# Performance work log

Measured on AMD Instinct MI355X. Metric: run time of the kernel, lower is better.

## Reference

```python
import jax, jax.numpy as jnp
import numpy as np

H, W, D, HEADS = 32, 32, 16, 8
EPS = 1e-5

def _ln(x, g, b):
    m = jnp.mean(x, -1, keepdims=True)
    v = jnp.mean((x - m) ** 2, -1, keepdims=True)
    return (x - m) / jnp.sqrt(v + EPS) * g + b

def _attn(x, w_qkv, w_proj, b_proj):
    # x: (Bb, N, C); torch Linear: y = x @ W.T + b
    Bb, N, C = x.shape
    hd = C // HEADS
    qkv = jnp.einsum('bnc,dc->bnd', x, w_qkv).reshape(Bb, N, 3, HEADS, hd)
    q, k, v = qkv[:, :, 0], qkv[:, :, 1], qkv[:, :, 2]  # (Bb,N,h,hd)
    att = jnp.einsum('bnhd,bmhd->bhnm', q, k) * (hd ** -0.5)
    att = jax.nn.softmax(att, axis=-1)
    o = jnp.einsum('bhnm,bmhd->bnhd', att, v).reshape(Bb, N, C)
    return jnp.einsum('bnc,dc->bnd', o, w_proj) + b_proj

def setup_inputs() -> dict:
    key = jax.random.key(0)
    ks = jax.random.split(key, 8)
    C, HID = 96, 384
    s = 0.02
    return {
        'x': jax.random.normal(ks[0], (1, C, D, H, W), jnp.float32),
        'norm1_g': jnp.ones((C,), jnp.float32),
        'norm1_b': jnp.zeros((C,), jnp.float32),
        'qkv_hw_w': jax.random.normal(ks[1], (3 * C, C), jnp.float32) * s,
        'proj_hw_w': jax.random.normal(ks[2], (C, C), jnp.float32) * s,
        'proj_hw_b': jnp.zeros((C,), jnp.float32),
        'qkv_t_w': jax.random.normal(ks[3], (3 * C, C), jnp.float32) * s,
        'proj_t_w': jax.random.normal(ks[4], (C, C), jnp.float32) * s,
        'proj_t_b': jnp.zeros((C,), jnp.float32),
        'norm2_g': jnp.ones((C,), jnp.float32),
        'norm2_b': jnp.zeros((C,), jnp.float32),
        'fc1_w': jax.random.normal(ks[5], (HID, C), jnp.float32) * s,
        'fc1_b': jnp.zeros((HID,), jnp.float32),
        'fc2_w': jax.random.normal(ks[6], (C, HID), jnp.float32) * s,
        'fc2_b': jnp.zeros((C,), jnp.float32),
    }

def reference(x, norm1_g, norm1_b, qkv_hw_w, proj_hw_w, proj_hw_b,
              qkv_t_w, proj_t_w, proj_t_b, norm2_g, norm2_b,
              fc1_w, fc1_b, fc2_w, fc2_b):
    B, C = x.shape[0], x.shape[1]
    HWn = H * W
    xf = x.reshape(B, C, -1).transpose(0, 2, 1)  # (B, L, C), L = D*H*W (D-major)
    shortcut = xf
    n1 = _ln(xf, norm1_g, norm1_b).reshape(B, D, HWn, C)
    # attention over H*W tokens (batched over B*D)
    a_hw = _attn(n1.reshape(B * D, HWn, C), qkv_hw_w, proj_hw_w, proj_hw_b)
    a_hw = a_hw.reshape(B, -1, C)  # D-major token order
    # attention over D tokens (batched over B*H*W)
    a_t = _attn(n1.transpose(0, 2, 1, 3).reshape(B * HWn, D, C), qkv_t_w, proj_t_w, proj_t_b)
    a_t = a_t.reshape(B, HWn * D, C)  # HW-major order (faithful to original view)
    out_res = shortcut + a_hw + a_t
    h1 = jax.nn.gelu(jnp.einsum('blc,hc->blh', _ln(out_res, norm2_g, norm2_b), fc1_w) + fc1_b,
                     approximate=False)
    mlp_out = jnp.einsum('blh,ch->blc', h1, fc2_w) + fc2_b
    out_ffn = out_res + mlp_out
    out = out_ffn.reshape(B, H, W, D, C).transpose(0, 4, 3, 1, 2)  # (B,C,D,H,W)
    return out
```

## Files before the change

kernel.cpp:

```cpp
#include <hip/hip_runtime.h>
#include <math.h>

#define L_TOK 16384
#define C_DIM 96
#define N_HEADS 8
#define HD 12
#define D_DIM 16
#define HW_N 1024
#define HID_DIM 384
#define SCALE 0.2886751345948129f
#define LOG2E 1.4426950408889634f

typedef _Float16 h4 __attribute__((ext_vector_type(4)));
typedef __fp16 fp16x2 __attribute__((ext_vector_type(2)));
typedef float v4f __attribute__((ext_vector_type(4)));

static __device__ __forceinline__ float fast_exp2(float x) {
#if __has_builtin(__builtin_amdgcn_exp2f)
    return __builtin_amdgcn_exp2f(x);
#else
    float r;
    asm("v_exp_f32 %0, %1" : "=v"(r) : "v"(x));
    return r;
#endif
}

static __device__ __forceinline__ h4 pack4(float a, float b, float c, float d) {
    fp16x2 lo = __builtin_amdgcn_cvt_pkrtz(a, b);
    fp16x2 hi = __builtin_amdgcn_cvt_pkrtz(c, d);
    union { fp16x2 p[2]; h4 v; } u;
    u.p[0] = lo; u.p[1] = hi;
    return u.v;
}

__global__ __launch_bounds__(256) void prep_kernel(
    const float* __restrict__ x, const float* __restrict__ g1,
    const float* __restrict__ b1, _Float16* __restrict__ n1h,
    const float* __restrict__ qkv_hw_w, const float* __restrict__ qkv_t_w,
    const float* __restrict__ proj_hw_w, const float* __restrict__ proj_t_w,
    const float* __restrict__ proj_hw_b, const float* __restrict__ proj_t_b,
    const float* __restrict__ fc1_w, const float* __restrict__ fc2_w,
    _Float16* __restrict__ wq, _Float16* __restrict__ wp,
    _Float16* __restrict__ wf1, _Float16* __restrict__ wf2,
    float* __restrict__ bp) {
    if (blockIdx.x < 64) {
        int l = blockIdx.x * 256 + threadIdx.x;
        float v[C_DIM];
        float s = 0.f;
#pragma unroll
        for (int c = 0; c < C_DIM; c++) {
            v[c] = x[(size_t)c * L_TOK + l];
            s += v[c];
        }
        float mean = s * (1.f / C_DIM);
        float var = 0.f;
#pragma unroll
        for (int c = 0; c < C_DIM; c++) {
            float dd = v[c] - mean;
            var += dd * dd;
        }
        float r = rsqrtf(var * (1.f / C_DIM) + 1e-5f);
        _Float16* op = n1h + (size_t)l * C_DIM;
#pragma unroll
        for (int c = 0; c < C_DIM; c += 4) {
            h4 o;
            o[0] = (_Float16)((v[c + 0] - mean) * r * g1[c + 0] + b1[c + 0]);
            o[1] = (_Float16)((v[c + 1] - mean) * r * g1[c + 1] + b1[c + 1]);
            o[2] = (_Float16)((v[c + 2] - mean) * r * g1[c + 2] + b1[c + 2]);
            o[3] = (_Float16)((v[c + 3] - mean) * r * g1[c + 3] + b1[c + 3]);
            *(h4*)(op + c) = o;
        }
        return;
    }
    int idx = (blockIdx.x - 64) * 256 + threadIdx.x;
    if (idx < 55296) {
        int n = idx / 96;
        float v = (n < 288) ? qkv_hw_w[idx] : qkv_t_w[idx - 27648];
        bool isq = (n < 96) || (n >= 288 && n < 384);
        wq[idx] = (_Float16)(isq ? v * (SCALE * LOG2E) : v);
    } else if (idx < 55296 + 18432) {
        int i = idx - 55296;
        int n = i / 192, k = i % 192;
        float v = (k < 96) ? proj_hw_w[n * 96 + k] : proj_t_w[n * 96 + k - 96];
        wp[i] = (_Float16)v;
    } else if (idx < 73728 + 36864) {
        int i = idx - 73728;
        wf1[i] = (_Float16)fc1_w[i];
    } else if (idx < 110592 + 36864) {
        int i = idx - 110592;
        wf2[i] = (_Float16)fc2_w[i];
    } else if (idx < 147456 + 96) {
        int i = idx - 147456;
        bp[i] = proj_hw_b[i] + proj_t_b[i];
    }
}

#define GBM 64
#define GBN 48
#define GBK 96
#define LSTRIDE 104

__global__ __launch_bounds__(256) void gemm_qkv(
    const _Float16* __restrict__ A, const _Float16* __restrict__ W,
    _Float16* __restrict__ Qp, _Float16* __restrict__ Kp,
    _Float16* __restrict__ VTp, _Float16* __restrict__ Tp) {
    __shared__ _Float16 As[GBM][LSTRIDE];
    __shared__ _Float16 Ws[GBN][LSTRIDE];
    const int t = threadIdx.x;
    const int m0 = blockIdx.x * GBM;
    const int n0 = blockIdx.y * GBN;
    const int lane = t & 63, w = t >> 6, g = lane >> 4, r = lane & 15;

    v4f acc[3];
#pragma unroll
    for (int nt = 0; nt < 3; nt++) {
        acc[nt][0] = 0.f; acc[nt][1] = 0.f; acc[nt][2] = 0.f; acc[nt][3] = 0.f;
    }
#pragma unroll
    for (int i = 0; i < 3; i++) {
        int idx = t + i * 256;
        int row = idx / 12, c = idx % 12;
        *(float4*)&As[row][c * 8] =
            *(const float4*)&A[(size_t)(m0 + row) * 96 + c * 8];
    }
#pragma unroll
    for (int i = 0; i < 3; i++) {
        int idx = t + i * 256;
        if (idx < 576) {
            int row = idx / 12, c = idx % 12;
            *(float4*)&Ws[row][c * 8] =
                *(const float4*)&W[(size_t)(n0 + row) * 96 + c * 8];
        }
    }
    __syncthreads();
#pragma unroll
    for (int ks = 0; ks < 6; ks++) {
        h4 af = *(const h4*)&As[w * 16 + r][ks * 16 + 4 * g];
#pragma unroll
        for (int nt = 0; nt < 3; nt++) {
            h4 wf = *(const h4*)&Ws[nt * 16 + r][ks * 16 + 4 * g];
            acc[nt] = __builtin_amdgcn_mfma_f32_16x16x16f16(wf, af, acc[nt], 0, 0, 0);
        }
    }

    const int m = m0 + w * 16 + r;
    const int d = m >> 10, hw = m & 1023;
    const int by = blockIdx.y;
#pragma unroll
    for (int nt = 0; nt < 3; nt++) {
        const int nb = n0 + nt * 16 + 4 * g;
        h4 ov;
        ov[0] = (_Float16)acc[nt][0]; ov[1] = (_Float16)acc[nt][1];
        ov[2] = (_Float16)acc[nt][2]; ov[3] = (_Float16)acc[nt][3];
        if (by < 2) {
            int n = nb;
            int h = (unsigned)n / 12u, dd = n - h * 12;
            *(h4*)&Qp[((size_t)(d * 8 + h) * 1024 + hw) * 12 + dd] = ov;
        } else if (by < 4) {
            int n = nb - 96;
            int h = (unsigned)n / 12u, dd = n - h * 12;
            *(h4*)&Kp[((size_t)(d * 8 + h) * 1024 + hw) * 12 + dd] = ov;
        } else if (by < 6) {
            int n = nb - 192;
            int h = (unsigned)n / 12u, dd = n - h * 12;
#pragma unroll
            for (int j = 0; j < 4; j++) {
                VTp[((size_t)(d * 8 + h) * 12 + dd + j) * 1024 + hw] = ov[j];
            }
        } else {
            *(h4*)&Tp[(size_t)(hw * 16 + d) * 288 + (nb - 288)] = ov;
        }
    }
}

__global__ __launch_bounds__(256) void fused_mlp(
    const _Float16* __restrict__ A, const _Float16* __restrict__ wp,
    const float* __restrict__ bp, const float* __restrict__ x,
    const float* __restrict__ g2, const float* __restrict__ b2,
    const _Float16* __restrict__ wf1, const float* __restrict__ f1b,
    const _Float16* __restrict__ wf2, const float* __restrict__ f2b,
    float* __restrict__ out) {
    __shared__ __align__(16) char pool[46592];
    _Float16* Abuf = (_Float16*)pool;
    _Float16* Wbuf = (_Float16*)(pool + 13312);
    _Float16* N2   = (_Float16*)(pool + 33280);
    float*    sh   = (float*)pool;

    const int t = threadIdx.x;
    const int bx = blockIdx.x;
    const int bxs = (bx & 7) * 32 + (bx >> 3);
    const int m0 = bxs * 64;
    const int lane = t & 63, w = t >> 6, g = lane >> 4, r = lane & 15;
    const int ml = w * 16 + r;
    const int m = m0 + ml;

    v4f acc[6];
#pragma unroll
    for (int nt = 0; nt < 6; nt++) {
        acc[nt][0] = 0.f; acc[nt][1] = 0.f; acc[nt][2] = 0.f; acc[nt][3] = 0.f;
    }
    for (int kc = 0; kc < 2; kc++) {
        __syncthreads();
#pragma unroll
        for (int i = 0; i < 3; i++) {
            int idx = t + i * 256;
            int row = idx / 12, c = idx % 12;
            *(float4*)&Abuf[row * LSTRIDE + c * 8] =
                *(const float4*)&A[(size_t)(m0 + row) * 192 + kc * 96 + c * 8];
        }
#pragma unroll
        for (int i = 0; i < 5; i++) {
            int idx = t + i * 256;
            if (idx < 1152) {
                int row = idx / 12, c = idx % 12;
                *(float4*)&Wbuf[row * LSTRIDE + c * 8] =
                    *(const float4*)&wp[(size_t)row * 192 + kc * 96 + c * 8];
            }
        }
        __syncthreads();
#pragma unroll
        for (int ks = 0; ks < 6; ks++) {
            h4 af = *(const h4*)&Abuf[ml * LSTRIDE + ks * 16 + 4 * g];
#pragma unroll
            for (int nt = 0; nt < 6; nt++) {
                h4 wf = *(const h4*)&Wbuf[(nt * 16 + r) * LSTRIDE + ks * 16 + 4 * g];
                acc[nt] =
                    __builtin_amdgcn_mfma_f32_16x16x16f16(wf, af, acc[nt], 0, 0, 0);
            }
        }
    }
    float v[24];
    float sum = 0.f;
#pragma unroll
    for (int nt = 0; nt < 6; nt++) {
        const int nb = nt * 16 + 4 * g;
        float4 bv = *(const float4*)&bp[nb];
        float a0 = acc[nt][0] + bv.x + x[(size_t)(nb + 0) * L_TOK + m];
        float a1 = acc[nt][1] + bv.y + x[(size_t)(nb + 1) * L_TOK + m];
        float a2 = acc[nt][2] + bv.z + x[(size_t)(nb + 2) * L_TOK + m];
        float a3 = acc[nt][3] + bv.w + x[(size_t)(nb + 3) * L_TOK + m];
        v[nt * 4 + 0] = a0; v[nt * 4 + 1] = a1;
        v[nt * 4 + 2] = a2; v[nt * 4 + 3] = a3;
        sum += (a0 + a1) + (a2 + a3);
    }
    sum += __shfl_xor(sum, 16, 64);
    sum += __shfl_xor(sum, 32, 64);
    float mean = sum * (1.f / 96.f);
    float ss = 0.f;
#pragma unroll
    for (int i = 0; i < 24; i++) {
        float dd = v[i] - mean;
        ss += dd * dd;
    }
    ss += __shfl_xor(ss, 16, 64);
    ss += __shfl_xor(ss, 32, 64);
    float rstd = rsqrtf(ss * (1.f / 96.f) + 1e-5f);
#pragma unroll
    for (int nt = 0; nt < 6; nt++) {
        const int nb = nt * 16 + 4 * g;
        float4 gg = *(const float4*)&g2[nb];
        float4 bb = *(const float4*)&b2[nb];
        h4 o;
        o[0] = (_Float16)((v[nt * 4 + 0] - mean) * rstd * gg.x + bb.x);
        o[1] = (_Float16)((v[nt * 4 + 1] - mean) * rstd * gg.y + bb.y);
        o[2] = (_Float16)((v[nt * 4 + 2] - mean) * rstd * gg.z + bb.z);
        o[3] = (_Float16)((v[nt * 4 + 3] - mean) * rstd * gg.w + bb.w);
        *(h4*)&N2[ml * LSTRIDE + nb] = o;
    }

    h4 hf[4][6];
    for (int nc = 0; nc < 4; nc++) {
        __syncthreads();
#pragma unroll
        for (int i = 0; i < 5; i++) {
            int idx = t + i * 256;
            if (idx < 1152) {
                int row = idx / 12, c = idx % 12;
                *(float4*)&Wbuf[row * LSTRIDE + c * 8] =
                    *(const float4*)&wf1[(size_t)(nc * 96 + row) * 96 + c * 8];
            }
        }
        __syncthreads();
        v4f f[6];
#pragma unroll
        for (int nt = 0; nt < 6; nt++) {
            f[nt][0] = 0.f; f[nt][1] = 0.f; f[nt][2] = 0.f; f[nt][3] = 0.f;
        }
#pragma unroll
        for (int ks = 0; ks < 6; ks++) {
            h4 af = *(const h4*)&N2[ml * LSTRIDE + ks * 16 + 4 * g];
#pragma unroll
            for (int nt = 0; nt < 6; nt++) {
                h4 wf = *(const h4*)&Wbuf[(nt * 16 + r) * LSTRIDE + ks * 16 + 4 * g];
                f[nt] = __builtin_amdgcn_mfma_f32_16x16x16f16(wf, af, f[nt], 0, 0, 0);
            }
        }
#pragma unroll
        for (int nt = 0; nt < 6; nt++) {
            const int nb = nc * 96 + nt * 16 + 4 * g;
            float4 bv = *(const float4*)&f1b[nb];
            float u0 = f[nt][0] + bv.x, u1 = f[nt][1] + bv.y;
            float u2 = f[nt][2] + bv.z, u3 = f[nt][3] + bv.w;
            h4 o;
            o[0] = (_Float16)(0.5f * u0 * (1.f + erff(u0 * 0.7071067811865476f)));
            o[1] = (_Float16)(0.5f * u1 * (1.f + erff(u1 * 0.7071067811865476f)));
            o[2] = (_Float16)(0.5f * u2 * (1.f + erff(u2 * 0.7071067811865476f)));
            o[3] = (_Float16)(0.5f * u3 * (1.f + erff(u3 * 0.7071067811865476f)));
            hf[nc][nt] = o;
        }
    }

    v4f o6[6];
#pragma unroll
    for (int nt = 0; nt < 6; nt++) {
        o6[nt][0] = 0.f; o6[nt][1] = 0.f; o6[nt][2] = 0.f; o6[nt][3] = 0.f;
    }
    for (int kc = 0; kc < 4; kc++) {
        __syncthreads();
#pragma unroll
        for (int i = 0; i < 5; i++) {
            int idx = t + i * 256;
            if (idx < 1152) {
                int row = idx / 12, c = idx % 12;
                *(float4*)&Wbuf[row * LSTRIDE + c * 8] =
                    *(const float4*)&wf2[(size_t)row * 384 + kc * 96 + c * 8];
            }
        }
        __syncthreads();
#pragma unroll
        for (int ks = 0; ks < 6; ks++) {
            h4 af = hf[kc][ks];
#pragma unroll
            for (int nt = 0; nt < 6; nt++) {
                h4 wf = *(const h4*)&Wbuf[(nt * 16 + r) * LSTRIDE + ks * 16 + 4 * g];
                o6[nt] = __builtin_amdgcn_mfma_f32_16x16x16f16(wf, af, o6[nt], 0, 0, 0);
            }
        }
    }

    __syncthreads();
#pragma unroll
    for (int nt = 0; nt < 6; nt++) {
        const int nb = nt * 16 + 4 * g;
        float4 bv = *(const float4*)&f2b[nb];
        sh[(nb + 0) * 68 + ml] = o6[nt][0] + bv.x + v[nt * 4 + 0];
        sh[(nb + 1) * 68 + ml] = o6[nt][1] + bv.y + v[nt * 4 + 1];
        sh[(nb + 2) * 68 + ml] = o6[nt][2] + bv.z + v[nt * 4 + 2];
        sh[(nb + 3) * 68 + ml] = o6[nt][3] + bv.w + v[nt * 4 + 3];
    }
    __syncthreads();
    const int hh = m0 >> 9, ww0 = (m0 >> 4) & 31;
#pragma unroll
    for (int i = 0; i < 6; i++) {
        int task = t + i * 256;
        int n = task >> 4, dd = task & 15;
        float4 ov;
        ov.x = sh[n * 68 + dd];
        ov.y = sh[n * 68 + dd + 16];
        ov.z = sh[n * 68 + dd + 32];
        ov.w = sh[n * 68 + dd + 48];
        *(float4*)&out[(size_t)n * L_TOK + dd * 1024 + hh * 32 + ww0] = ov;
    }
}

__global__ __launch_bounds__(256) void attn_hw_kernel(
    const _Float16* __restrict__ Qp, const _Float16* __restrict__ Kp,
    const _Float16* __restrict__ VTp, _Float16* __restrict__ o_cat) {
    __shared__ _Float16 K_lds[1024 * 12];
    __shared__ _Float16 VT_lds[13 * 1032];
    const int t = threadIdx.x;
    const int qb = blockIdx.x, h = blockIdx.y, d = blockIdx.z;
    const size_t tokbase = (size_t)d * HW_N;
    const int hoff = h * HD;
    const size_t slice = (size_t)(d * 8 + h);

    {
        const float4* Kg = (const float4*)(Kp + slice * 12288);
        float4* K4 = (float4*)K_lds;
#pragma unroll
        for (int i = 0; i < 6; i++) K4[t + i * 256] = Kg[t + i * 256];
        const float4* Vg = (const float4*)(VTp + slice * 12288);
#pragma unroll
        for (int i = 0; i < 6; i++) {
            int off = t + i * 256;
            int row = off >> 7, col = (off & 127) * 8;
            *(float4*)&VT_lds[row * 1032 + col] = Vg[off];
        }
        unsigned* zp = (unsigned*)&VT_lds[12 * 1032];
        zp[t] = 0x3C003C00u; zp[t + 256] = 0x3C003C00u;
        if (t < 4) zp[t + 512] = 0x3C003C00u;
    }

    const int lane = t & 63, w = t >> 6, g = lane >> 4, r = lane & 15;
    const int q0w = qb * 128 + w * 32;

    h4 zf; zf[0] = zf[1] = zf[2] = zf[3] = (_Float16)0.f;
    h4 qf[2];
    {
        const _Float16* Qbase = Qp + (slice * 1024 + q0w + r) * 12 + 4 * g;
#pragma unroll
        for (int qt = 0; qt < 2; qt++) {
            qf[qt] = (g < 3) ? *(const h4*)(Qbase + qt * 16 * 12) : zf;
        }
    }

    v4f acc[2];
#pragma unroll
    for (int qt = 0; qt < 2; qt++) {
        acc[qt][0] = acc[qt][1] = acc[qt][2] = acc[qt][3] = 0.f;
    }

    const int koff = r * 12 + 4 * g;
    const int rowc = (r < 12) ? r : 12;
    const int voff = rowc * 1032 + 4 * g;

    __syncthreads();

    v4f zero; zero[0] = zero[1] = zero[2] = zero[3] = 0.f;
#pragma unroll 4
    for (int kt = 0; kt < HW_N / 16; kt++) {
        h4 kf = (g < 3) ? *(const h4*)&K_lds[kt * 192 + koff] : zf;
        h4 vf = *(const h4*)&VT_lds[voff + kt * 16];
#pragma unroll
        for (int qt = 0; qt < 2; qt++) {
            v4f s = __builtin_amdgcn_mfma_f32_16x16x16f16(kf, qf[qt], zero, 0, 0, 0);
            h4 pf = pack4(fast_exp2(s[0]), fast_exp2(s[1]),
                          fast_exp2(s[2]), fast_exp2(s[3]));
            acc[qt] = __builtin_amdgcn_mfma_f32_16x16x16f16(vf, pf, acc[qt], 0, 0, 0);
        }
    }

#pragma unroll
    for (int qt = 0; qt < 2; qt++) {
        float denom = __shfl(acc[qt][0], 48 + r, 64);
        float rs = 1.f / denom;
        if (g < 3) {
            _Float16* op =
                o_cat + (tokbase + q0w + qt * 16 + r) * 192 + hoff + 4 * g;
            h4 o;
            o[0] = (_Float16)(acc[qt][0] * rs);
            o[1] = (_Float16)(acc[qt][1] * rs);
            o[2] = (_Float16)(acc[qt][2] * rs);
            o[3] = (_Float16)(acc[qt][3] * rs);
            *(h4*)op = o;
        }
    }
}

__global__ __launch_bounds__(256) void attn_t_kernel(
    const _Float16* __restrict__ Tp, _Float16* __restrict__ o_cat) {
    int gid = blockIdx.x * 256 + threadIdx.x;
    int hw = gid >> 7;
    int h = (gid >> 4) & 7;
    int q = gid & 15;
    const int hoff = h * HD;
    const _Float16* base = Tp + (size_t)(hw * 16) * 288;

    float qr[HD];
    {
        const _Float16* p = base + q * 288 + hoff;
        h4 a = *(const h4*)p, b = *(const h4*)(p + 4), c = *(const h4*)(p + 8);
#pragma unroll
        for (int e = 0; e < 4; e++) {
            qr[e] = (float)a[e]; qr[4 + e] = (float)b[e]; qr[8 + e] = (float)c[e];
        }
    }
    float s[D_DIM];
    float mx = -1e30f;
#pragma unroll
    for (int j = 0; j < D_DIM; j++) {
        const _Float16* kp = base + j * 288 + 96 + hoff;
        h4 a = *(const h4*)kp, b = *(const h4*)(kp + 4), c = *(const h4*)(kp + 8);
        float dot = 0.f;
#pragma unroll
        for (int e = 0; e < 4; e++) {
            dot += qr[e] * (float)a[e] + qr[4 + e] * (float)b[e] +
                   qr[8 + e] * (float)c[e];
        }
        s[j] = dot;
        mx = fmaxf(mx, dot);
    }
    float sum = 0.f;
#pragma unroll
    for (int j = 0; j < D_DIM; j++) {
        s[j] = fast_exp2(s[j] - mx);
        sum += s[j];
    }
    float rs = 1.f / sum;
    float o[HD];
#pragma unroll
    for (int e = 0; e < HD; e++) o[e] = 0.f;
#pragma unroll
    for (int j = 0; j < D_DIM; j++) {
        const _Float16* vp = base + j * 288 + 192 + hoff;
        h4 a = *(const h4*)vp, b = *(const h4*)(vp + 4), c = *(const h4*)(vp + 8);
        float p = s[j];
#pragma unroll
        for (int e = 0; e < 4; e++) {
            o[e] += p * (float)a[e];
            o[4 + e] += p * (float)b[e];
            o[8 + e] += p * (float)c[e];
        }
    }
    _Float16* op = o_cat + ((size_t)hw * D_DIM + q) * 192 + 96 + hoff;
#pragma unroll
    for (int e = 0; e < HD; e += 4) {
        h4 a;
        a[0] = (_Float16)(o[e] * rs); a[1] = (_Float16)(o[e + 1] * rs);
        a[2] = (_Float16)(o[e + 2] * rs); a[3] = (_Float16)(o[e + 3] * rs);
        *(h4*)(op + e) = a;
    }
}

extern "C" void kernel_launch(void* const* d_in, const int* in_sizes, int n_in,
                              void* d_out, int out_size, void* d_ws,
                              size_t ws_size, hipStream_t stream) {
    const float* x         = (const float*)d_in[0];
    const float* norm1_g   = (const float*)d_in[1];
    const float* norm1_b   = (const float*)d_in[2];
    const float* qkv_hw_w  = (const float*)d_in[3];
    const float* proj_hw_w = (const float*)d_in[4];
    const float* proj_hw_b = (const float*)d_in[5];
    const float* qkv_t_w   = (const float*)d_in[6];
    const float* proj_t_w  = (const float*)d_in[7];
    const float* proj_t_b  = (const float*)d_in[8];
    const float* norm2_g   = (const float*)d_in[9];
    const float* norm2_b   = (const float*)d_in[10];
    const float* fc1_w     = (const float*)d_in[11];
    const float* fc1_b     = (const float*)d_in[12];
    const float* fc2_w     = (const float*)d_in[13];
    const float* fc2_b     = (const float*)d_in[14];
    float* out = (float*)d_out;

    char* ws = (char*)d_ws;
    _Float16* n1h    = (_Float16*)ws;
    _Float16* o_cat  = n1h + (size_t)L_TOK * C_DIM;
    float*    out_res= (float*)(o_cat + (size_t)L_TOK * 192);
    _Float16* packs  = (_Float16*)(out_res + (size_t)L_TOK * C_DIM);
    _Float16* Qp     = packs;
    _Float16* Kp     = Qp + 1572864;
    _Float16* VTp    = Kp + 1572864;
    _Float16* Tp     = VTp + 1572864;
    _Float16* wq     = Tp + (size_t)L_TOK * 288;
    _Float16* wp     = wq + 55296;
    _Float16* wf1    = wp + 18432;
    _Float16* wf2    = wf1 + 36864;
    float*    bp     = (float*)(wf2 + 36864);

    prep_kernel<<<641, 256, 0, stream>>>(x, norm1_g, norm1_b, n1h,
                                         qkv_hw_w, qkv_t_w, proj_hw_w,
                                         proj_t_w, proj_hw_b, proj_t_b,
                                         fc1_w, fc2_w, wq, wp, wf1, wf2, bp);
    gemm_qkv<<<dim3(L_TOK / GBM, 576 / GBN), 256, 0, stream>>>(
        n1h, wq, Qp, Kp, VTp, Tp);
    attn_hw_kernel<<<dim3(8, N_HEADS, D_DIM), 256, 0, stream>>>(
        Qp, Kp, VTp, o_cat);
    attn_t_kernel<<<(HW_N * N_HEADS * D_DIM) / 256, 256, 0, stream>>>(Tp, o_cat);
    fused_mlp<<<L_TOK / 64, 256, 0, stream>>>(
        o_cat, wp, bp, x, norm2_g, norm2_b, wf1, fc1_b, wf2, fc2_b, out);
}
```

Baseline: 93.99 us.

## Read MLP weights and activations directly from global memory, dropping LDS staging

The fused MLP kernel no longer stages activation and weight tiles through shared memory with barriers. MFMA operands now come straight from global memory, which relies on L1/L2 caching of the small weight matrices, and the LayerNorm output is kept in registers. Shared memory is cut to the output transpose buffer and the per-chunk __syncthreads are removed. The aim is to remove barrier stalls and LDS traffic and raise occupancy, at the cost of many more uncoalesced global loads and possibly more register pressure from full unrolling.

```diff
diff --git a/kernel.cpp b/kernel.cpp
--- a/kernel.cpp
+++ b/kernel.cpp
@@ -180,11 +180,7 @@
     const _Float16* __restrict__ wf1, const float* __restrict__ f1b,
     const _Float16* __restrict__ wf2, const float* __restrict__ f2b,
     float* __restrict__ out) {
-    __shared__ __align__(16) char pool[46592];
-    _Float16* Abuf = (_Float16*)pool;
-    _Float16* Wbuf = (_Float16*)(pool + 13312);
-    _Float16* N2   = (_Float16*)(pool + 33280);
-    float*    sh   = (float*)pool;
+    __shared__ float sh[96 * 68];
 
     const int t = threadIdx.x;
     const int bx = blockIdx.x;
@@ -199,33 +195,21 @@
     for (int nt = 0; nt < 6; nt++) {
         acc[nt][0] = 0.f; acc[nt][1] = 0.f; acc[nt][2] = 0.f; acc[nt][3] = 0.f;
     }
+#pragma unroll
     for (int kc = 0; kc < 2; kc++) {
-        __syncthreads();
-#pragma unroll
-        for (int i = 0; i < 3; i++) {
-            int idx = t + i * 256;
-            int row = idx / 12, c = idx % 12;
-            *(float4*)&Abuf[row * LSTRIDE + c * 8] =
-                *(const float4*)&A[(size_t)(m0 + row) * 192 + kc * 96 + c * 8];
-        }
-#pragma unroll
-        for (int i = 0; i < 5; i++) {
-            int idx = t + i * 256;
-            if (idx < 1152) {
-                int row = idx / 12, c = idx % 12;
-                *(float4*)&Wbuf[row * LSTRIDE + c * 8] =
-                    *(const float4*)&wp[(size_t)row * 192 + kc * 96 + c * 8];
-            }
-        }
-        __syncthreads();
+        h4 af[6];
 #pragma unroll
         for (int ks = 0; ks < 6; ks++) {
-            h4 af = *(const h4*)&Abuf[ml * LSTRIDE + ks * 16 + 4 * g];
+            af[ks] = *(const h4*)&A[(size_t)m * 192 + kc * 96 + ks * 16 + 4 * g];
+        }
+#pragma unroll
+        for (int ks = 0; ks < 6; ks++) {
 #pragma unroll
             for (int nt = 0; nt < 6; nt++) {
-                h4 wf = *(const h4*)&Wbuf[(nt * 16 + r) * LSTRIDE + ks * 16 + 4 * g];
+                h4 wf = *(const h4*)&wp[(size_t)(nt * 16 + r) * 192 + kc * 96 +
+                                        ks * 16 + 4 * g];
                 acc[nt] =
-                    __builtin_amdgcn_mfma_f32_16x16x16f16(wf, af, acc[nt], 0, 0, 0);
+                    __builtin_amdgcn_mfma_f32_16x16x16f16(wf, af[ks], acc[nt], 0, 0, 0);
             }
         }
     }
@@ -255,32 +239,21 @@
     ss += __shfl_xor(ss, 16, 64);
     ss += __shfl_xor(ss, 32, 64);
     float rstd = rsqrtf(ss * (1.f / 96.f) + 1e-5f);
+    h4 n2f[6];
 #pragma unroll
     for (int nt = 0; nt < 6; nt++) {
         const int nb = nt * 16 + 4 * g;
         float4 gg = *(const float4*)&g2[nb];
         float4 bb = *(const float4*)&b2[nb];
-        h4 o;
-        o[0] = (_Float16)((v[nt * 4 + 0] - mean) * rstd * gg.x + bb.x);
-        o[1] = (_Float16)((v[nt * 4 + 1] - mean) * rstd * gg.y + bb.y);
-        o[2] = (_Float16)((v[nt * 4 + 2] - mean) * rstd * gg.z + bb.z);
-        o[3] = (_Float16)((v[nt * 4 + 3] - mean) * rstd * gg.w + bb.w);
-        *(h4*)&N2[ml * LSTRIDE + nb] = o;
+        n2f[nt] = pack4((v[nt * 4 + 0] - mean) * rstd * gg.x + bb.x,
+                        (v[nt * 4 + 1] - mean) * rstd * gg.y + bb.y,
+                        (v[nt * 4 + 2] - mean) * rstd * gg.z + bb.z,
+                        (v[nt * 4 + 3] - mean) * rstd * gg.w + bb.w);
     }
 
     h4 hf[4][6];
+#pragma unroll
     for (int nc = 0; nc < 4; nc++) {
-        __syncthreads();
-#pragma unroll
-        for (int i = 0; i < 5; i++) {
-            int idx = t + i * 256;
-            if (idx < 1152) {
-                int row = idx / 12, c = idx % 12;
-                *(float4*)&Wbuf[row * LSTRIDE + c * 8] =
-                    *(const float4*)&wf1[(size_t)(nc * 96 + row) * 96 + c * 8];
-            }
-        }
-        __syncthreads();
         v4f f[6];
 #pragma unroll
         for (int nt = 0; nt < 6; nt++) {
@@ -288,11 +261,12 @@
         }
 #pragma unroll
         for (int ks = 0; ks < 6; ks++) {
-            h4 af = *(const h4*)&N2[ml * LSTRIDE + ks * 16 + 4 * g];
 #pragma unroll
             for (int nt = 0; nt < 6; nt++) {
-                h4 wf = *(const h4*)&Wbuf[(nt * 16 + r) * LSTRIDE + ks * 16 + 4 * g];
-                f[nt] = __builtin_amdgcn_mfma_f32_16x16x16f16(wf, af, f[nt], 0, 0, 0);
+                h4 wf = *(const h4*)&wf1[(size_t)(nc * 96 + nt * 16 + r) * 96 +
+                                         ks * 16 + 4 * g];
+                f[nt] =
+                    __builtin_amdgcn_mfma_f32_16x16x16f16(wf, n2f[ks], f[nt], 0, 0, 0);
             }
         }
 #pragma unroll
@@ -301,12 +275,11 @@
             float4 bv = *(const float4*)&f1b[nb];
             float u0 = f[nt][0] + bv.x, u1 = f[nt][1] + bv.y;
             float u2 = f[nt][2] + bv.z, u3 = f[nt][3] + bv.w;
-            h4 o;
-            o[0] = (_Float16)(0.5f * u0 * (1.f + erff(u0 * 0.7071067811865476f)));
-            o[1] = (_Float16)(0.5f * u1 * (1.f + erff(u1 * 0.7071067811865476f)));
-            o[2] = (_Float16)(0.5f * u2 * (1.f + erff(u2 * 0.7071067811865476f)));
-            o[3] = (_Float16)(0.5f * u3 * (1.f + erff(u3 * 0.7071067811865476f)));
-            hf[nc][nt] = o;
+            hf[nc][nt] =
+                pack4(0.5f * u0 * (1.f + erff(u0 * 0.7071067811865476f)),
+                      0.5f * u1 * (1.f + erff(u1 * 0.7071067811865476f)),
+                      0.5f * u2 * (1.f + erff(u2 * 0.7071067811865476f)),
+                      0.5f * u3 * (1.f + erff(u3 * 0.7071067811865476f)));
         }
     }
 
@@ -315,30 +288,20 @@
     for (int nt = 0; nt < 6; nt++) {
         o6[nt][0] = 0.f; o6[nt][1] = 0.f; o6[nt][2] = 0.f; o6[nt][3] = 0.f;
     }
+#pragma unroll
     for (int kc = 0; kc < 4; kc++) {
-        __syncthreads();
-#pragma unroll
-        for (int i = 0; i < 5; i++) {
-            int idx = t + i * 256;
-            if (idx < 1152) {
-                int row = idx / 12, c = idx % 12;
-                *(float4*)&Wbuf[row * LSTRIDE + c * 8] =
-                    *(const float4*)&wf2[(size_t)row * 384 + kc * 96 + c * 8];
+#pragma unroll
+        for (int ks = 0; ks < 6; ks++) {
+#pragma unroll
+            for (int nt = 0; nt < 6; nt++) {
+                h4 wf = *(const h4*)&wf2[(size_t)(nt * 16 + r) * 384 + kc * 96 +
+                                         ks * 16 + 4 * g];
+                o6[nt] =
+                    __builtin_amdgcn_mfma_f32_16x16x16f16(wf, hf[kc][ks], o6[nt], 0, 0, 0);
             }
         }
-        __syncthreads();
-#pragma unroll
-        for (int ks = 0; ks < 6; ks++) {
-            h4 af = hf[kc][ks];
-#pragma unroll
-            for (int nt = 0; nt < 6; nt++) {
-                h4 wf = *(const h4*)&Wbuf[(nt * 16 + r) * LSTRIDE + ks * 16 + 4 * g];
-                o6[nt] = __builtin_amdgcn_mfma_f32_16x16x16f16(wf, af, o6[nt], 0, 0, 0);
-            }
-        }
-    }
-
-    __syncthreads();
+    }
+
 #pragma unroll
     for (int nt = 0; nt < 6; nt++) {
         const int nb = nt * 16 + 4 * g;
```

New measurement: 116.6 us. 24.1% more time.
